# Kernel optimization log

Measured on AMD Instinct MI355X. Metric: run time of the kernel, lower is better.

Reference implementation:

```python
import jax, jax.numpy as jnp
import numpy as np

B, NQ, D, H, L, P, FFN = 32, 300, 256, 8, 3, 4, 1024
SPATIAL = [(80, 80), (40, 40), (20, 20)]  # static multi-scale feature shapes (640px, strides 8/16/32)
S = sum(h * w for h, w in SPATIAL)  # 8400
HD = D // H


def _ln(x, g, b, eps=1e-5):
    m = jnp.mean(x, -1, keepdims=True)
    v = jnp.mean((x - m) ** 2, -1, keepdims=True)
    return (x - m) * jax.lax.rsqrt(v + eps) * g + b


def _grid_sample(img, grid):
    # img: (N,C,Hh,Ww); grid: (N,Q,Pp,2) in [-1,1]; bilinear, zeros padding, align_corners=False
    N, C, Hh, Ww = img.shape
    x = (grid[..., 0] + 1.0) * (Ww * 0.5) - 0.5
    y = (grid[..., 1] + 1.0) * (Hh * 0.5) - 0.5
    x0 = jnp.floor(x)
    y0 = jnp.floor(y)
    wx1 = x - x0
    wy1 = y - y0
    x0i = x0.astype(jnp.int32)
    y0i = y0.astype(jnp.int32)
    flat = img.reshape(N, C, Hh * Ww)
    Q, Pp = grid.shape[1], grid.shape[2]

    def corner(xi, yi, w):
        valid = (xi >= 0) & (xi < Ww) & (yi >= 0) & (yi < Hh)
        idx = jnp.clip(yi, 0, Hh - 1) * Ww + jnp.clip(xi, 0, Ww - 1)
        v = jnp.take_along_axis(flat, idx.reshape(N, 1, Q * Pp), axis=2).reshape(N, C, Q, Pp)
        return v * (w * valid)[:, None]

    return (corner(x0i, y0i, (1 - wx1) * (1 - wy1))
            + corner(x0i + 1, y0i, wx1 * (1 - wy1))
            + corner(x0i, y0i + 1, (1 - wx1) * wy1)
            + corner(x0i + 1, y0i + 1, wx1 * wy1))


def setup_inputs() -> dict:
    key = jax.random.key(0)
    ks = iter(jax.random.split(key, 32))
    inp = {
        'hidden_states': jax.random.normal(next(ks), (B, NQ, D), jnp.float32),
        'position_embeddings': jax.random.normal(next(ks), (B, NQ, D), jnp.float32),
        'reference_points': jax.random.uniform(next(ks), (B, NQ, 1, 4), jnp.float32, 0.1, 0.9),
        'encoder_hidden_states': jax.random.normal(next(ks), (B, S, D), jnp.float32),
    }
    for name, shape in [('Wq', (D, D)), ('Wk', (D, D)), ('Wv', (D, D)), ('Wo', (D, D)),
                        ('Woff', (D, H * L * P * 2)), ('Waw', (D, H * L * P)),
                        ('Wval', (D, D)), ('Wout', (D, D)), ('W1', (D, FFN)), ('W2', (FFN, D))]:
        inp[name] = jax.random.normal(next(ks), shape, jnp.float32) * 0.02
    for name, dim in [('bq', D), ('bk', D), ('bv', D), ('bo', D), ('boff', H * L * P * 2),
                      ('baw', H * L * P), ('bval', D), ('bout', D), ('b1', FFN), ('b2', D)]:
        inp[name] = jnp.zeros((dim,), jnp.float32)
    for g, bname in [('ln1_g', 'ln1_b'), ('ln2_g', 'ln2_b'), ('ln3_g', 'ln3_b')]:
        inp[g] = jnp.ones((D,), jnp.float32)
        inp[bname] = jnp.zeros((D,), jnp.float32)
    return inp


def reference(hidden_states, position_embeddings, reference_points, encoder_hidden_states,
              Wq, bq, Wk, bk, Wv, bv, Wo, bo, ln1_g, ln1_b,
              Woff, boff, Waw, baw, Wval, bval, Wout, bout, ln2_g, ln2_b,
              W1, b1, W2, b2, ln3_g, ln3_b):
    hs = hidden_states
    # ---- self attention (pos-embedded q/k, raw v) ----
    hp = hs + position_embeddings
    q = ((hp @ Wq + bq) * (HD ** -0.5)).reshape(B, NQ, H, HD)
    k = (hp @ Wk + bk).reshape(B, NQ, H, HD)
    v = (hs @ Wv + bv).reshape(B, NQ, H, HD)
    attn = jax.nn.softmax(jnp.einsum('bqhd,bkhd->bhqk', q, k), axis=-1)
    sa = jnp.einsum('bhqk,bkhd->bqhd', attn, v).reshape(B, NQ, D) @ Wo + bo
    hs = _ln(hs + sa, ln1_g, ln1_b)
    # ---- multi-scale deformable cross attention ----
    hp = hs + position_embeddings
    value = (encoder_hidden_states @ Wval + bval).reshape(B, S, H, HD)
    off = (hp @ Woff + boff).reshape(B, NQ, H, L, P, 2)
    aw = jax.nn.softmax((hp @ Waw + baw).reshape(B, NQ, H, L * P), axis=-1).reshape(B, NQ, H, L, P)
    ref = reference_points  # (B,NQ,1,4) boxes -> 4-coord branch
    loc = ref[:, :, None, :, None, :2] + off / P * ref[:, :, None, :, None, 2:] * 0.5
    grids = (2.0 * loc - 1.0).transpose(0, 2, 1, 3, 4, 5).reshape(B * H, NQ, L, P, 2)
    start = 0
    samples = []
    for lvl, (hh, ww) in enumerate(SPATIAL):
        v_l = value[:, start:start + hh * ww]  # (B,hw,H,HD)
        start += hh * ww
        v_l = v_l.transpose(0, 2, 3, 1).reshape(B * H, HD, hh, ww)
        samples.append(_grid_sample(v_l, grids[:, :, lvl]))  # (B*H,HD,NQ,P)
    sampled = jnp.stack(samples, axis=3).reshape(B * H, HD, NQ, L * P)
    w = aw.transpose(0, 2, 1, 3, 4).reshape(B * H, 1, NQ, L * P)
    ca = (sampled * w).sum(-1).reshape(B, H * HD, NQ).transpose(0, 2, 1) @ Wout + bout
    hs = _ln(hs + ca, ln2_g, ln2_b)
    # ---- FFN ----
    ff = jax.nn.relu(hs @ W1 + b1) @ W2 + b2
    return _ln(hs + ff, ln3_g, ln3_b)
```

## Files before the change

### kernel.cpp

```cpp
#include <hip/hip_runtime.h>
#include <hip/hip_bf16.h>

typedef unsigned int  uint32;
typedef unsigned short ushort16;
typedef __bf16 bfx8 __attribute__((ext_vector_type(8)));
typedef float  f32x4 __attribute__((ext_vector_type(4)));

typedef __attribute__((address_space(1))) const unsigned int gas_u32;
typedef __attribute__((address_space(3))) unsigned int las_u32;

#define B_   32
#define NQ_  300
#define D_   256
#define H_   8
#define HD_  32
#define L_   3
#define P_   4
#define S_   8400
#define FFN_ 1024
#define M1   (B_*NQ_)
#define MV   (B_*S_)
#define NQP  320
#define NQT  19

__device__ inline ushort16 f2bf(float x) {
  uint32 u = __float_as_uint(x);
  uint32 r = u + 0x7fffu + ((u >> 16) & 1u);
  return (ushort16)(r >> 16);
}
__device__ inline uint32 cvtpk(float lo, float hi) {
  uint32 r; asm("v_cvt_pk_bf16_f32 %0, %1, %2" : "=v"(r) : "v"(lo), "v"(hi)); return r;
}

struct WPrep {
  const float* src[9];
  ushort16*    dst[9];
  int K[9], N[9], Npad[9], tileEnd[9];
  float scale[9];
  const float* wval; ushort16* wvalc;
  const float* bqs;  const float* bks;  float* bqk;
  const float* boffs; const float* baws; float* boffaw;
};

__global__ __launch_bounds__(256) void rt_wprep(WPrep a)
{
  __shared__ float t[32][33];
  int blk = blockIdx.x;
  if (blk < 904) {
    int wi = 0;
    while (blk >= a.tileEnd[wi]) wi++;
    int base = wi ? a.tileEnd[wi - 1] : 0;
    int idx = blk - base;
    int K = a.K[wi], N = a.N[wi];
    int ntx = a.Npad[wi] / 32;
    int n0 = (idx % ntx) * 32, k0 = (idx / ntx) * 32;
    float sc = a.scale[wi];
    const float* W = a.src[wi];
    ushort16* WT = a.dst[wi];
    int c = threadIdx.x & 31, r = threadIdx.x >> 5;
#pragma unroll
    for (int i = 0; i < 4; i++) {
      int nn = n0 + c;
      t[r + i * 8][c] = (nn < N) ? W[(size_t)(k0 + r + i * 8) * N + nn] : 0.f;
    }
    __syncthreads();
#pragma unroll
    for (int i = 0; i < 4; i++)
      WT[(size_t)(n0 + r + i * 8) * K + k0 + c] = f2bf(t[c][r + i * 8] * sc);
  } else if (blk < 936) {
    int gid = (blk - 904) * 256 + threadIdx.x;
    int c = gid >> 8, n = gid & 255;
    const float* W = a.wval;
    uint4 u;
    u.x = (uint32)f2bf(W[(c*8+0)*256 + n]) | ((uint32)f2bf(W[(c*8+1)*256 + n]) << 16);
    u.y = (uint32)f2bf(W[(c*8+2)*256 + n]) | ((uint32)f2bf(W[(c*8+3)*256 + n]) << 16);
    u.z = (uint32)f2bf(W[(c*8+4)*256 + n]) | ((uint32)f2bf(W[(c*8+5)*256 + n]) << 16);
    u.w = (uint32)f2bf(W[(c*8+6)*256 + n]) | ((uint32)f2bf(W[(c*8+7)*256 + n]) << 16);
    *(uint4*)&a.wvalc[(size_t)c * 2048 + n * 8] = u;
  } else if (blk == 936) {
    a.bqk[threadIdx.x] = a.bqs[threadIdx.x] * a.scale[0];
  } else if (blk == 937) {
    a.bqk[256 + threadIdx.x] = a.bks[threadIdx.x];
  } else if (blk == 938) {
    if (threadIdx.x < 192) a.boffaw[threadIdx.x] = a.boffs[threadIdx.x];
  } else {
    if (threadIdx.x < 96) a.boffaw[192 + threadIdx.x] = a.baws[threadIdx.x];
  }
}

__global__ __launch_bounds__(1024) void rt_vgemm(
    const float* __restrict__ A, const ushort16* __restrict__ BC,
    const float* __restrict__ bias, ushort16* __restrict__ Vout)
{
  __shared__ __align__(16) char ldsB[65536];
  const int tid = threadIdx.x;
  const int lane = tid & 63, w = tid >> 6;
  const int l15 = lane & 15, l4 = lane >> 4;
  const int cid = blockIdx.x >> 8;
  const int rg  = blockIdx.x & 255;

#pragma unroll
  for (int i = 0; i < 4; ++i) {
    int g = tid * 16 + i * 16384;
    int kc = g >> 11;
    __builtin_amdgcn_global_load_lds(
        (gas_u32*)(const void*)((const char*)BC + g + (kc + cid) * 2048),
        (las_u32*)(void*)(&ldsB[g]), 16, 0, 0);
  }
  __syncthreads();

  const int wrow = w * 16 + l15;
  const float* Abase = A + (size_t)wrow * 256 + l4 * 8;

  for (int t = rg; t < MV / 256; t += 256) {
    const float* Ap = Abase + (size_t)t * 65536;
    f32x4 acc[8];
#pragma unroll
    for (int i = 0; i < 8; ++i) acc[i] = (f32x4){0.f, 0.f, 0.f, 0.f};

    f32x4 c0 = *(const f32x4*)(Ap);
    f32x4 c1 = *(const f32x4*)(Ap + 4);
#pragma unroll
    for (int ts = 0; ts < 8; ++ts) {
      f32x4 n0, n1;
      if (ts < 7) {
        n0 = *(const f32x4*)(Ap + (ts + 1) * 32);
        n1 = *(const f32x4*)(Ap + (ts + 1) * 32 + 4);
      }
      uint4 u;
      u.x = cvtpk(c0[0], c0[1]); u.y = cvtpk(c0[2], c0[3]);
      u.z = cvtpk(c1[0], c1[1]); u.w = cvtpk(c1[2], c1[3]);
      bfx8 af = __builtin_bit_cast(bfx8, u);
      const char* bp = &ldsB[(ts * 4 + l4) * 2048 + l15 * 16];
#pragma unroll
      for (int ni = 0; ni < 8; ++ni) {
        bfx8 bg = *(const bfx8*)(const void*)(bp + ni * 256);
        acc[ni] = __builtin_amdgcn_mfma_f32_16x16x32_bf16(bg, af, acc[ni], 0, 0, 0);
      }
      c0 = n0; c1 = n1;
    }

    int row = t * 256 + wrow;
    int bb = row / S_, s = row - bb * S_;
    ushort16* vb = Vout + (((size_t)bb * H_) * S_ + s) * HD_;
#pragma unroll
    for (int ni = 0; ni < 8; ++ni) {
      int col = cid * 128 + ni * 16 + l4 * 4;
      f32x4 bv = *(const f32x4*)(bias + col);
      int hh = col >> 5, hd = col & 31;
      uint2 st;
      st.x = cvtpk(acc[ni][0] + bv[0], acc[ni][1] + bv[1]);
      st.y = cvtpk(acc[ni][2] + bv[2], acc[ni][3] + bv[3]);
      *(uint2*)(vb + (size_t)hh * S_ * HD_ + hd) = st;
    }
  }
}

#define GBM 128
#define GBN 128
#define GBK 32
#define LDP 40

__global__ __launch_bounds__(256) void rt_mgemm(
    const float* __restrict__ A, const float* __restrict__ A2,
    const ushort16* __restrict__ BT, const float* __restrict__ bias,
    float* __restrict__ C,
    ushort16* __restrict__ Sc, ushort16* __restrict__ Sc2,
    int M, int N, int K, float scale, int mode)
{
  __shared__ __align__(16) ushort16 As[GBM][LDP];
  __shared__ __align__(16) ushort16 Bs[GBN][LDP];
  const int tid  = threadIdx.x;
  const int lane = tid & 63;
  const int w    = tid >> 6;
  const int wr   = (w >> 1) * 64;
  const int wc   = (w & 1) * 64;
  const int bm   = blockIdx.y * GBM;
  const int bn   = blockIdx.x * GBN;
  const int l15  = lane & 15;
  const int l4   = lane >> 4;

  f32x4 acc[4][4];
#pragma unroll
  for (int i = 0; i < 4; i++)
#pragma unroll
    for (int j = 0; j < 4; j++)
      acc[i][j] = (f32x4){0.f, 0.f, 0.f, 0.f};

  const int arow = tid >> 3, akc = tid & 7;
  const int brow = tid >> 2, bkc = tid & 3;

  for (int k0 = 0; k0 < K; k0 += GBK) {
#pragma unroll
    for (int i = 0; i < 4; i++) {
      int row = arow + i * 32;
      f32x4 v = *(const f32x4*)(A + (size_t)(bm + row) * K + k0 + akc * 4);
      if (A2) {
        f32x4 v2 = *(const f32x4*)(A2 + (size_t)(bm + row) * K + k0 + akc * 4);
#pragma unroll
        for (int r = 0; r < 4; r++) v[r] += v2[r];
      }
      uint2 u;
      u.x = cvtpk(v.x, v.y);
      u.y = cvtpk(v.z, v.w);
      *(uint2*)(&As[row][akc * 4]) = u;
    }
#pragma unroll
    for (int i = 0; i < 2; i++) {
      int row = brow + i * 64;
      uint4 v = *(const uint4*)(BT + (size_t)(bn + row) * K + k0 + bkc * 8);
      *(uint4*)(&Bs[row][bkc * 8]) = v;
    }
    __syncthreads();

    bfx8 af[4], bg[4];
#pragma unroll
    for (int mi = 0; mi < 4; mi++)
      af[mi] = *(const bfx8*)(&As[wr + mi * 16 + l15][l4 * 8]);
#pragma unroll
    for (int ni = 0; ni < 4; ni++)
      bg[ni] = *(const bfx8*)(&Bs[wc + ni * 16 + l15][l4 * 8]);
#pragma unroll
    for (int mi = 0; mi < 4; mi++)
#pragma unroll
      for (int ni = 0; ni < 4; ni++)
        acc[mi][ni] = __builtin_amdgcn_mfma_f32_16x16x32_bf16(af[mi], bg[ni], acc[mi][ni], 0, 0, 0);
    __syncthreads();
  }

#pragma unroll
  for (int mi = 0; mi < 4; mi++) {
#pragma unroll
    for (int ni = 0; ni < 4; ni++) {
      int col = bn + wc + ni * 16 + l15;
      if (col >= N) continue;
      float bv = bias[col];
#pragma unroll
      for (int r = 0; r < 4; r++) {
        int row = bm + wr + mi * 16 + l4 * 4 + r;
        float vv = (acc[mi][ni][r] + bv) * scale;
        if (mode == 1) vv = fmaxf(vv, 0.f);
        if (mode == 3) {
          int bb = row / NQ_, q = row - bb * NQ_;
          int hh = col >> 5, hd = col & 31;
          Sc[(((size_t)bb * H_ + hh) * NQP + q) * HD_ + hd] = f2bf(vv);
        } else if (mode == 4) {
          int bb = row / NQ_, q = row - bb * NQ_;
          int hh = col >> 5, hd = col & 31;
          ushort16* d = (hh < 8) ? Sc : Sc2;
          d[(((size_t)bb * H_ + (hh & 7)) * NQP + q) * HD_ + hd] = f2bf(vv);
        } else {
          C[(size_t)row * N + col] = vv;
        }
      }
    }
  }
}

__global__ __launch_bounds__(256) void rt_vtr(const ushort16* __restrict__ vh,
                                              ushort16* __restrict__ vt)
{
  __shared__ ushort16 t[64][33];
  int bh = blockIdx.x;
  const ushort16* src = vh + (size_t)bh * NQP * HD_;
  ushort16* dst = vt + (size_t)bh * HD_ * NQP;
  int tid = threadIdx.x;
  int lrow = tid >> 2, lc8 = (tid & 3) * 8;
  int ohd = tid >> 3, oq8 = (tid & 7) * 8;
  for (int r0 = 0; r0 < NQP; r0 += 64) {
    uint4 v = {0u, 0u, 0u, 0u};
    if (r0 + lrow < NQ_)
      v = *(const uint4*)(src + (size_t)(r0 + lrow) * HD_ + lc8);
    ushort16* tp = &t[lrow][lc8];
    tp[0] = (ushort16)(v.x & 0xffff); tp[1] = (ushort16)(v.x >> 16);
    tp[2] = (ushort16)(v.y & 0xffff); tp[3] = (ushort16)(v.y >> 16);
    tp[4] = (ushort16)(v.z & 0xffff); tp[5] = (ushort16)(v.z >> 16);
    tp[6] = (ushort16)(v.w & 0xffff); tp[7] = (ushort16)(v.w >> 16);
    __syncthreads();
    uint4 o;
    o.x = (uint32)t[oq8 + 0][ohd] | ((uint32)t[oq8 + 1][ohd] << 16);
    o.y = (uint32)t[oq8 + 2][ohd] | ((uint32)t[oq8 + 3][ohd] << 16);
    o.z = (uint32)t[oq8 + 4][ohd] | ((uint32)t[oq8 + 5][ohd] << 16);
    o.w = (uint32)t[oq8 + 6][ohd] | ((uint32)t[oq8 + 7][ohd] << 16);
    *(uint4*)(dst + (size_t)ohd * NQP + r0 + oq8) = o;
    __syncthreads();
  }
}

__global__ __launch_bounds__(256) void rt_fattn(
    const ushort16* __restrict__ qh, const ushort16* __restrict__ kh,
    const ushort16* __restrict__ vt, float* __restrict__ O)
{
  int gw  = blockIdx.x * 4 + (threadIdx.x >> 6);
  int bh  = gw / NQT, qt = gw - bh * NQT;
  int b   = bh >> 3, h = bh & 7;
  int lane = threadIdx.x & 63;
  int l15 = lane & 15, l4 = lane >> 4;
  int kb4 = l4 * 4;
  const ushort16* Qb = qh + (size_t)bh * NQP * HD_;
  const ushort16* Kb = kh + (size_t)bh * NQP * HD_;
  const ushort16* Vb = vt + (size_t)bh * HD_ * NQP;
  int q = qt * 16 + l15;

  bfx8 bgQ = *(const bfx8*)(const void*)(Qb + (size_t)q * HD_ + l4 * 8);
  f32x4 o0 = {0.f,0.f,0.f,0.f}, o1 = {0.f,0.f,0.f,0.f};
  float m = -1e30f, ssum = 0.f;

  for (int k0 = 0; k0 < NQP; k0 += 32) {
    bfx8 afk0 = *(const bfx8*)(const void*)(Kb + (size_t)(k0 + l15) * HD_ + l4 * 8);
    bfx8 afk1 = *(const bfx8*)(const void*)(Kb + (size_t)(k0 + 16 + l15) * HD_ + l4 * 8);
    f32x4 z = {0.f,0.f,0.f,0.f};
    f32x4 s0 = __builtin_amdgcn_mfma_f32_16x16x32_bf16(afk0, bgQ, z, 0, 0, 0);
    f32x4 s1 = __builtin_amdgcn_mfma_f32_16x16x32_bf16(afk1, bgQ, z, 0, 0, 0);
    int ka = k0 + kb4, kbb = k0 + 16 + kb4;
#pragma unroll
    for (int r = 0; r < 4; r++) {
      if (ka  + r >= NQ_) s0[r] = -1e30f;
      if (kbb + r >= NQ_) s1[r] = -1e30f;
    }
    float cm = fmaxf(fmaxf(fmaxf(s0[0], s0[1]), fmaxf(s0[2], s0[3])),
                     fmaxf(fmaxf(s1[0], s1[1]), fmaxf(s1[2], s1[3])));
    cm = fmaxf(cm, __shfl_xor(cm, 16));
    cm = fmaxf(cm, __shfl_xor(cm, 32));
    float nm = fmaxf(m, cm);
    float sc = __expf(m - nm);
    m = nm;
    f32x4 p0, p1;
#pragma unroll
    for (int r = 0; r < 4; r++) { p0[r] = __expf(s0[r] - m); p1[r] = __expf(s1[r] - m); }
    float ls = (p0[0]+p0[1]+p0[2]+p0[3]) + (p1[0]+p1[1]+p1[2]+p1[3]);
    ls += __shfl_xor(ls, 16);
    ls += __shfl_xor(ls, 32);
    ssum = ssum * sc + ls;

    uint32 t0w0 = cvtpk(p0[0], p0[1]);
    uint32 t0w1 = cvtpk(p0[2], p0[3]);
    uint32 t1w0 = cvtpk(p1[0], p1[1]);
    uint32 t1w1 = cvtpk(p1[2], p1[3]);
    int srcA = l15 + 32 * (l4 & 1);
    int srcB = srcA + 16;
    uint32 a00 = __shfl((int)t0w0, srcA), a01 = __shfl((int)t0w1, srcA);
    uint32 b00 = __shfl((int)t0w0, srcB), b01 = __shfl((int)t0w1, srcB);
    uint32 a10 = __shfl((int)t1w0, srcA), a11 = __shfl((int)t1w1, srcA);
    uint32 b10 = __shfl((int)t1w0, srcB), b11 = __shfl((int)t1w1, srcB);
    bool hi = (l4 >= 2);
    uint4 pw;
    pw.x = hi ? a10 : a00;
    pw.y = hi ? a11 : a01;
    pw.z = hi ? b10 : b00;
    pw.w = hi ? b11 : b01;
    bfx8 bgP = __builtin_bit_cast(bfx8, pw);

    bfx8 afv0 = *(const bfx8*)(const void*)(Vb + (size_t)l15 * NQP + k0 + l4 * 8);
    bfx8 afv1 = *(const bfx8*)(const void*)(Vb + (size_t)(16 + l15) * NQP + k0 + l4 * 8);
#pragma unroll
    for (int r = 0; r < 4; r++) { o0[r] *= sc; o1[r] *= sc; }
    o0 = __builtin_amdgcn_mfma_f32_16x16x32_bf16(afv0, bgP, o0, 0, 0, 0);
    o1 = __builtin_amdgcn_mfma_f32_16x16x32_bf16(afv1, bgP, o1, 0, 0, 0);
  }

  if (q < NQ_) {
    float inv = 1.f / ssum;
    float* op = O + ((size_t)(b * NQ_ + q)) * D_ + h * HD_ + kb4;
    f32x4 r0, r1;
#pragma unroll
    for (int r = 0; r < 4; r++) { r0[r] = o0[r] * inv; r1[r] = o1[r] * inv; }
    *(f32x4*)op = r0;
    *(f32x4*)(op + 16) = r1;
  }
}

__global__ __launch_bounds__(256) void rt_ln2(
    const float* __restrict__ X, const float* __restrict__ R1,
    const float* __restrict__ R2,
    const float* __restrict__ g, const float* __restrict__ be,
    float* __restrict__ O, int rows)
{
  int row = blockIdx.x * 4 + (threadIdx.x >> 6);
  int lane = threadIdx.x & 63;
  if (row >= rows) return;
  size_t base = (size_t)row * D_ + lane * 4;
  float4 x = *(const float4*)(X + base);
  float4 r = *(const float4*)(R1 + base);
  float v0 = x.x + r.x, v1 = x.y + r.y, v2 = x.z + r.z, v3 = x.w + r.w;
  if (R2) {
    float4 r2 = *(const float4*)(R2 + base);
    v0 += r2.x; v1 += r2.y; v2 += r2.z; v3 += r2.w;
  }
  float s = v0 + v1 + v2 + v3;
  float sq = v0*v0 + v1*v1 + v2*v2 + v3*v3;
#pragma unroll
  for (int o = 32; o >= 1; o >>= 1) { s += __shfl_xor(s, o); sq += __shfl_xor(sq, o); }
  float mean = s * (1.f / D_);
  float var  = sq * (1.f / D_) - mean * mean;
  float inv  = 1.f / sqrtf(var + 1e-5f);
  int c = lane * 4;
  float4 gv = *(const float4*)(g + c);
  float4 bv = *(const float4*)(be + c);
  float4 o4;
  o4.x = (v0 - mean) * inv * gv.x + bv.x;
  o4.y = (v1 - mean) * inv * gv.y + bv.y;
  o4.z = (v2 - mean) * inv * gv.z + bv.z;
  o4.w = (v3 - mean) * inv * gv.w + bv.w;
  *(float4*)(O + base) = o4;
}

__device__ inline void rt_acc8(const ushort16* p, float wgt, float* acc) {
  uint4 v = *(const uint4*)(const void*)p;
  acc[0] += wgt * __uint_as_float(v.x << 16);
  acc[1] += wgt * __uint_as_float(v.x & 0xffff0000u);
  acc[2] += wgt * __uint_as_float(v.y << 16);
  acc[3] += wgt * __uint_as_float(v.y & 0xffff0000u);
  acc[4] += wgt * __uint_as_float(v.z << 16);
  acc[5] += wgt * __uint_as_float(v.z & 0xffff0000u);
  acc[6] += wgt * __uint_as_float(v.w << 16);
  acc[7] += wgt * __uint_as_float(v.w & 0xffff0000u);
}

__global__ __launch_bounds__(256) void rt_deform(
    const ushort16* __restrict__ value,
    const float* __restrict__ offaw,
    const float* __restrict__ ref,
    float* __restrict__ O)
{
  int gid = blockIdx.x * 256 + threadIdx.x;
  int hd0 = (gid & 3) * 8;
  int bqh = gid >> 2;
  int h   = bqh & 7;
  int bq  = bqh >> 3;
  int b   = bq / NQ_;
  const float* rp = ref + (size_t)bq * 4;
  float rx = rp[0], ry = rp[1];
  float rw = rp[2] * 0.125f, rh = rp[3] * 0.125f;
  const float* op = offaw + (size_t)bq * 288 + h * 24;
  const float* ap = offaw + (size_t)bq * 288 + 192 + h * 12;
  float e[12]; float mx = -1e30f;
#pragma unroll
  for (int i = 0; i < 12; i++) { e[i] = ap[i]; mx = fmaxf(mx, e[i]); }
  float ssum = 0.f;
#pragma unroll
  for (int i = 0; i < 12; i++) { e[i] = __expf(e[i] - mx); ssum += e[i]; }
  float sinv = 1.f / ssum;

  const ushort16* vb = value + ((size_t)b * H_ + h) * (size_t)S_ * HD_ + hd0;
  float acc[8];
#pragma unroll
  for (int i = 0; i < 8; i++) acc[i] = 0.f;
  const int starts[3] = {0, 6400, 8000};
  const int dims[3]   = {80, 40, 20};
#pragma unroll
  for (int l = 0; l < L_; l++) {
    const int Wl = dims[l];
    const ushort16* vl = vb + (size_t)starts[l] * HD_;
#pragma unroll
    for (int p = 0; p < P_; p++) {
      int ip = l * P_ + p;
      float wgt = e[ip] * sinv;
      float x = (rx + op[ip*2+0] * rw) * Wl - 0.5f;
      float y = (ry + op[ip*2+1] * rh) * Wl - 0.5f;
      float x0f = floorf(x), y0f = floorf(y);
      int   x0 = (int)x0f,  y0 = (int)y0f;
      float wx1 = x - x0f, wy1 = y - y0f;
      float wx0 = 1.f - wx1, wy0 = 1.f - wy1;
      bool xok0 = (x0 >= 0) & (x0 < Wl), xok1 = (x0+1 >= 0) & (x0+1 < Wl);
      bool yok0 = (y0 >= 0) & (y0 < Wl), yok1 = (y0+1 >= 0) & (y0+1 < Wl);
      const ushort16* r0p = vl + (size_t)(y0 * Wl) * HD_;
      const ushort16* r1p = r0p + (size_t)Wl * HD_;
      if (xok0 & yok0) rt_acc8(r0p + (size_t)x0 * HD_,     wgt * wx0 * wy0, acc);
      if (xok1 & yok0) rt_acc8(r0p + (size_t)(x0+1) * HD_, wgt * wx1 * wy0, acc);
      if (xok0 & yok1) rt_acc8(r1p + (size_t)x0 * HD_,     wgt * wx0 * wy1, acc);
      if (xok1 & yok1) rt_acc8(r1p + (size_t)(x0+1) * HD_, wgt * wx1 * wy1, acc);
    }
  }
  float* outp = O + (size_t)bq * D_ + h * HD_ + hd0;
  float4 a0, a1;
  a0.x = acc[0]; a0.y = acc[1]; a0.z = acc[2]; a0.w = acc[3];
  a1.x = acc[4]; a1.y = acc[5]; a1.z = acc[6]; a1.w = acc[7];
  *(float4*)outp = a0;
  *(float4*)(outp + 4) = a1;
}

extern "C" void kernel_launch(void* const* d_in, const int* in_sizes, int n_in,
                              void* d_out, int out_size, void* d_ws, size_t ws_size,
                              hipStream_t stream)
{
  const float* hs   = (const float*)d_in[0];
  const float* pos  = (const float*)d_in[1];
  const float* ref  = (const float*)d_in[2];
  const float* ehs  = (const float*)d_in[3];
  const float* Wq   = (const float*)d_in[4];
  const float* Wk   = (const float*)d_in[5];
  const float* Wv   = (const float*)d_in[6];
  const float* Wo   = (const float*)d_in[7];
  const float* Woff = (const float*)d_in[8];
  const float* Waw  = (const float*)d_in[9];
  const float* Wval = (const float*)d_in[10];
  const float* Wout = (const float*)d_in[11];
  const float* W1   = (const float*)d_in[12];
  const float* W2   = (const float*)d_in[13];
  const float* bq   = (const float*)d_in[14];
  const float* bk   = (const float*)d_in[15];
  const float* bvv  = (const float*)d_in[16];
  const float* bo   = (const float*)d_in[17];
  const float* boff = (const float*)d_in[18];
  const float* baw  = (const float*)d_in[19];
  const float* bval = (const float*)d_in[20];
  const float* bout = (const float*)d_in[21];
  const float* b1   = (const float*)d_in[22];
  const float* b2   = (const float*)d_in[23];
  const float* ln1g = (const float*)d_in[24];
  const float* ln1b = (const float*)d_in[25];
  const float* ln2g = (const float*)d_in[26];
  const float* ln2b = (const float*)d_in[27];
  const float* ln3g = (const float*)d_in[28];
  const float* ln3b = (const float*)d_in[29];
  float* out = (float*)d_out;

  float* ws = (float*)d_ws;
  ushort16* value = (ushort16*)ws;
  float* t0     = ws + 36864000;
  float* t1     = ws + 39321600;
  float* hs1    = ws + 41779200;
  float* hs2    = ws + 44236800;
  float* offawb = ws + 46694400;
  float* ffn1   = ws + 49459200;
  ushort16* qh = (ushort16*)(ws + 59289600);
  ushort16* kh = (ushort16*)(ws + 60600320);
  ushort16* vh = (ushort16*)(ws + 61911040);
  ushort16* vt = (ushort16*)(ws + 63221760);
  ushort16* wbase  = (ushort16*)(ws + 64532480);
  ushort16* WqkT   = wbase;
  ushort16* WvT    = WqkT   + 131072;
  ushort16* WoT    = WvT    + 65536;
  ushort16* WoffawT= WoT    + 65536;
  ushort16* WoutT  = WoffawT+ 98304;
  ushort16* W1T    = WoutT  + 65536;
  ushort16* W2T    = W1T    + 262144;
  ushort16* WvalC  = W2T    + 262144;
  float* bqk    = (float*)(WvalC + 65536);
  float* boffaw = bqk + 512;

  const float qscale = 0.17677669529663687f;

  WPrep a;
  a.src[0]=Wq;   a.dst[0]=WqkT;            a.K[0]=256;  a.N[0]=256;  a.Npad[0]=256; a.scale[0]=qscale;
  a.src[1]=Wk;   a.dst[1]=WqkT+65536;      a.K[1]=256;  a.N[1]=256;  a.Npad[1]=256; a.scale[1]=1.f;
  a.src[2]=Wv;   a.dst[2]=WvT;             a.K[2]=256;  a.N[2]=256;  a.Npad[2]=256; a.scale[2]=1.f;
  a.src[3]=Wo;   a.dst[3]=WoT;             a.K[3]=256;  a.N[3]=256;  a.Npad[3]=256; a.scale[3]=1.f;
  a.src[4]=Woff; a.dst[4]=WoffawT;         a.K[4]=256;  a.N[4]=192;  a.Npad[4]=192; a.scale[4]=1.f;
  a.src[5]=Waw;  a.dst[5]=WoffawT+49152;   a.K[5]=256;  a.N[5]=96;   a.Npad[5]=96;  a.scale[5]=1.f;
  a.src[6]=Wout; a.dst[6]=WoutT;           a.K[6]=256;  a.N[6]=256;  a.Npad[6]=256; a.scale[6]=1.f;
  a.src[7]=W1;   a.dst[7]=W1T;             a.K[7]=256;  a.N[7]=1024; a.Npad[7]=1024;a.scale[7]=1.f;
  a.src[8]=W2;   a.dst[8]=W2T;             a.K[8]=1024; a.N[8]=256;  a.Npad[8]=256; a.scale[8]=1.f;
  int cum = 0;
  int tiles[9] = {64, 64, 64, 64, 48, 24, 64, 256, 256};
  for (int i = 0; i < 9; i++) { cum += tiles[i]; a.tileEnd[i] = cum; }
  a.wval = Wval; a.wvalc = WvalC;
  a.bqs = bq; a.bks = bk; a.bqk = bqk;
  a.boffs = boff; a.baws = baw; a.boffaw = boffaw;
  rt_wprep<<<dim3(940), 256, 0, stream>>>(a);

  rt_vgemm<<<dim3(512), 1024, 0, stream>>>(ehs, WvalC, bval, value);

  rt_mgemm<<<dim3(4, M1/GBM), 256, 0, stream>>>(hs, pos, WqkT, bqk, nullptr, qh, kh, M1, 512, 256, 1.f, 4);
  rt_mgemm<<<dim3(2, M1/GBM), 256, 0, stream>>>(hs, nullptr, WvT, bvv, nullptr, vh, nullptr, M1, 256, 256, 1.f, 3);
  rt_vtr<<<dim3(B_*H_), 256, 0, stream>>>(vh, vt);
  rt_fattn<<<dim3(B_*H_*NQT/4), 256, 0, stream>>>(qh, kh, vt, t0);
  rt_mgemm<<<dim3(2, M1/GBM), 256, 0, stream>>>(t0, nullptr, WoT, bo, t1, nullptr, nullptr, M1, 256, 256, 1.f, 0);
  rt_ln2<<<dim3(M1/4), 256, 0, stream>>>(hs, t1, nullptr, ln1g, ln1b, hs1, M1);
  rt_mgemm<<<dim3(3, M1/GBM), 256, 0, stream>>>(hs1, pos, WoffawT, boffaw, offawb, nullptr, nullptr, M1, 288, 256, 1.f, 0);
  rt_deform<<<dim3(M1*H_*4/256), 256, 0, stream>>>(value, offawb, ref, t0);
  rt_mgemm<<<dim3(2, M1/GBM), 256, 0, stream>>>(t0, nullptr, WoutT, bout, t1, nullptr, nullptr, M1, 256, 256, 1.f, 0);
  rt_ln2<<<dim3(M1/4), 256, 0, stream>>>(hs1, t1, nullptr, ln2g, ln2b, hs2, M1);
  rt_mgemm<<<dim3(8, M1/GBM), 256, 0, stream>>>(hs2, nullptr, W1T, b1, ffn1, nullptr, nullptr, M1, FFN_, 256, 1.f, 1);
  rt_mgemm<<<dim3(2, M1/GBM), 256, 0, stream>>>(ffn1, nullptr, W2T, b2, t1, nullptr, nullptr, M1, 256, 1024, 1.f, 0);
  rt_ln2<<<dim3(M1/4), 256, 0, stream>>>(hs2, t1, nullptr, ln3g, ln3b, out, M1);
}
```

Measured before the change: 446.0 us.

## Make value-projection GEMM blocks compute all 256 columns to read the A input once

The value projection GEMM now has each block hold the whole 256-column bf16 weight in 128KB of LDS and compute every output column, instead of splitting the columns across two blocks that each reread the fp32 activation rows. Blocks shrink to 512 threads, each tile covers 128 rows, and 256 persistent blocks are launched. All eight K-slices of A are loaded into registers up front in place of the old one-step prefetch. This halves global reads of the large encoder activations, but it doubles accumulator register use and LDS per block, which may lower occupancy and weaken latency hiding.

```diff
diff --git a/kernel.cpp b/kernel.cpp
--- a/kernel.cpp
+++ b/kernel.cpp
@@ -88,64 +88,59 @@
   }
 }
 
-__global__ __launch_bounds__(1024) void rt_vgemm(
+__global__ __launch_bounds__(512) void rt_vgemm(
     const float* __restrict__ A, const ushort16* __restrict__ BC,
     const float* __restrict__ bias, ushort16* __restrict__ Vout)
 {
-  __shared__ __align__(16) char ldsB[65536];
+  __shared__ __align__(16) char ldsB[131072];
   const int tid = threadIdx.x;
   const int lane = tid & 63, w = tid >> 6;
   const int l15 = lane & 15, l4 = lane >> 4;
-  const int cid = blockIdx.x >> 8;
-  const int rg  = blockIdx.x & 255;
-
-#pragma unroll
-  for (int i = 0; i < 4; ++i) {
-    int g = tid * 16 + i * 16384;
-    int kc = g >> 11;
+
+#pragma unroll
+  for (int i = 0; i < 16; ++i)
     __builtin_amdgcn_global_load_lds(
-        (gas_u32*)(const void*)((const char*)BC + g + (kc + cid) * 2048),
-        (las_u32*)(void*)(&ldsB[g]), 16, 0, 0);
-  }
+        (gas_u32*)(const void*)((const char*)BC + tid * 16 + i * 8192),
+        (las_u32*)(void*)(&ldsB[tid * 16 + i * 8192]), 16, 0, 0);
   __syncthreads();
 
   const int wrow = w * 16 + l15;
   const float* Abase = A + (size_t)wrow * 256 + l4 * 8;
 
-  for (int t = rg; t < MV / 256; t += 256) {
-    const float* Ap = Abase + (size_t)t * 65536;
-    f32x4 acc[8];
-#pragma unroll
-    for (int i = 0; i < 8; ++i) acc[i] = (f32x4){0.f, 0.f, 0.f, 0.f};
-
-    f32x4 c0 = *(const f32x4*)(Ap);
-    f32x4 c1 = *(const f32x4*)(Ap + 4);
+  for (int t = blockIdx.x; t < MV / 128; t += 256) {
+    const float* Ap = Abase + (size_t)t * 32768;
+    f32x4 Lr[16];
+#pragma unroll
+    for (int s = 0; s < 8; ++s) {
+      Lr[2 * s]     = *(const f32x4*)(Ap + s * 32);
+      Lr[2 * s + 1] = *(const f32x4*)(Ap + s * 32 + 4);
+    }
+    f32x4 acc[16];
+#pragma unroll
+    for (int i = 0; i < 16; ++i) acc[i] = (f32x4){0.f, 0.f, 0.f, 0.f};
+
 #pragma unroll
     for (int ts = 0; ts < 8; ++ts) {
-      f32x4 n0, n1;
-      if (ts < 7) {
-        n0 = *(const f32x4*)(Ap + (ts + 1) * 32);
-        n1 = *(const f32x4*)(Ap + (ts + 1) * 32 + 4);
-      }
       uint4 u;
-      u.x = cvtpk(c0[0], c0[1]); u.y = cvtpk(c0[2], c0[3]);
-      u.z = cvtpk(c1[0], c1[1]); u.w = cvtpk(c1[2], c1[3]);
+      u.x = cvtpk(Lr[2*ts][0], Lr[2*ts][1]);
+      u.y = cvtpk(Lr[2*ts][2], Lr[2*ts][3]);
+      u.z = cvtpk(Lr[2*ts+1][0], Lr[2*ts+1][1]);
+      u.w = cvtpk(Lr[2*ts+1][2], Lr[2*ts+1][3]);
       bfx8 af = __builtin_bit_cast(bfx8, u);
-      const char* bp = &ldsB[(ts * 4 + l4) * 2048 + l15 * 16];
-#pragma unroll
-      for (int ni = 0; ni < 8; ++ni) {
+      const char* bp = &ldsB[(ts * 4 + l4) * 4096 + l15 * 16];
+#pragma unroll
+      for (int ni = 0; ni < 16; ++ni) {
         bfx8 bg = *(const bfx8*)(const void*)(bp + ni * 256);
         acc[ni] = __builtin_amdgcn_mfma_f32_16x16x32_bf16(bg, af, acc[ni], 0, 0, 0);
       }
-      c0 = n0; c1 = n1;
-    }
-
-    int row = t * 256 + wrow;
+    }
+
+    int row = t * 128 + wrow;
     int bb = row / S_, s = row - bb * S_;
     ushort16* vb = Vout + (((size_t)bb * H_) * S_ + s) * HD_;
 #pragma unroll
-    for (int ni = 0; ni < 8; ++ni) {
-      int col = cid * 128 + ni * 16 + l4 * 4;
+    for (int ni = 0; ni < 16; ++ni) {
+      int col = ni * 16 + l4 * 4;
       f32x4 bv = *(const f32x4*)(bias + col);
       int hh = col >> 5, hd = col & 31;
       uint2 st;
@@ -560,7 +555,7 @@
   a.boffs = boff; a.baws = baw; a.boffaw = boffaw;
   rt_wprep<<<dim3(940), 256, 0, stream>>>(a);
 
-  rt_vgemm<<<dim3(512), 1024, 0, stream>>>(ehs, WvalC, bval, value);
+  rt_vgemm<<<dim3(256), 512, 0, stream>>>(ehs, WvalC, bval, value);
 
   rt_mgemm<<<dim3(4, M1/GBM), 256, 0, stream>>>(hs, pos, WqkT, bqk, nullptr, qh, kh, M1, 512, 256, 1.f, 4);
   rt_mgemm<<<dim3(2, M1/GBM), 256, 0, stream>>>(hs, nullptr, WvT, bvv, nullptr, vh, nullptr, M1, 256, 256, 1.f, 3);
```

After: 400.5 us. 1.11x faster.
